# Optimization experiments

Hardware: AMD Instinct MI355X
Metric: run time of the kernel (lower is better)

Reference implementation:

```python
import jax, jax.numpy as jnp
import numpy as np

IN_DIM, H1, H2, H3, LATENT = 1024, 1024, 512, 256, 256
D, K, BETA = 32, 2048, 0.25
B = 16384


def _leaky(x):
    return jax.nn.leaky_relu(x, negative_slope=0.01)


def setup_inputs() -> dict:
    key = jax.random.key(0)
    ks = jax.random.split(key, 18)
    def lin(k, fan_in, fan_out):
        kw, kb = jax.random.split(k)
        s = 1.0 / np.sqrt(fan_in)
        W = jax.random.uniform(kw, (fan_in, fan_out), jnp.float32, -s, s)
        b = jax.random.uniform(kb, (fan_out,), jnp.float32, -s, s)
        return W, b
    We1, be1 = lin(ks[0], IN_DIM, H1)
    We2, be2 = lin(ks[1], H1, H2)
    We3, be3 = lin(ks[2], H2, H3)
    We4, be4 = lin(ks[3], H3, LATENT)
    Wd1, bd1 = lin(ks[4], LATENT, H3)
    Wd2, bd2 = lin(ks[5], H3, H2)
    Wd3, bd3 = lin(ks[6], H2, H1)
    Wd4, bd4 = lin(ks[7], H1, IN_DIM)
    E = jax.random.uniform(ks[8], (K, D), jnp.float32, -1.0 / K, 1.0 / K)  # codebook
    x = jax.random.uniform(ks[9], (B, IN_DIM), jnp.float32)
    return {"x": x, "We1": We1, "be1": be1, "We2": We2, "be2": be2,
            "We3": We3, "be3": be3, "We4": We4, "be4": be4, "E": E,
            "Wd1": Wd1, "bd1": bd1, "Wd2": Wd2, "bd2": bd2,
            "Wd3": Wd3, "bd3": bd3, "Wd4": Wd4, "bd4": bd4}


def reference(x, We1, be1, We2, be2, We3, be3, We4, be4, E,
              Wd1, bd1, Wd2, bd2, Wd3, bd3, Wd4, bd4):
    # encoder MLP
    h = _leaky(x @ We1 + be1)
    h = _leaky(h @ We2 + be2)
    h = _leaky(h @ We3 + be3)
    z = h @ We4 + be4                      # [B, LATENT]
    # vector quantizer
    zr = z.reshape(-1, D)                  # [N, D], N = B*LATENT/D
    dist = (jnp.sum(zr * zr, axis=1, keepdims=True)
            + jnp.sum(E * E, axis=1)
            - 2.0 * zr @ E.T)              # [N, K]
    idx = jnp.argmin(dist, axis=1)         # [N]
    # one-hot @ E == direct gather of nearest codebook rows
    q = E[idx].reshape(z.shape)            # [B, LATENT]
    commit = jnp.mean(jnp.sum(jnp.square(jax.lax.stop_gradient(q) - z), axis=1))
    embed = jnp.mean(jnp.sum(jnp.square(q - jax.lax.stop_gradient(z)), axis=1))
    vq_loss = BETA * commit + embed
    e = z + jax.lax.stop_gradient(q - z)   # straight-through
    # decoder MLP
    h = _leaky(e @ Wd1 + bd1)
    h = _leaky(h @ Wd2 + bd2)
    h = _leaky(h @ Wd3 + bd3)
    recon = jax.nn.sigmoid(h @ Wd4 + bd4)
    recon_loss = jnp.mean(jnp.sum(jnp.square(recon - x), axis=-1))
    loss = recon_loss + vq_loss
    return z, e, recon, loss, recon_loss, vq_loss
```

## Files before the change

### kernel.cpp

```cpp
#include <hip/hip_runtime.h>
#include <stdint.h>

typedef __attribute__((ext_vector_type(8))) _Float16 half8;
typedef __attribute__((ext_vector_type(4))) _Float16 half4;
typedef __attribute__((ext_vector_type(4))) float f32x4;

__device__ __forceinline__ void gload_lds16(const void* g, void* l) {
  __builtin_amdgcn_global_load_lds(
      (const __attribute__((address_space(1))) void*)g,
      (__attribute__((address_space(3))) void*)l, 16, 0, 0);
}

#define GBAR asm volatile("s_barrier" ::: "memory")
#define LGKM0                                            \
  asm volatile("s_waitcnt lgkmcnt(0)" ::: "memory");     \
  __builtin_amdgcn_sched_barrier(0)

#define MMA_Q(QM, QN)                                                        \
  __builtin_amdgcn_s_setprio(1);                                             \
  _Pragma("unroll") for (int s = 0; s < 2; s++)                              \
  _Pragma("unroll") for (int i = 0; i < 4; i++)                              \
  _Pragma("unroll") for (int j = 0; j < 2; j++)                              \
      acc[(QM) * 4 + i][(QN) * 2 + j] = __builtin_amdgcn_mfma_f32_16x16x32_f16( \
          af[i][s], bq[j][s], acc[(QM) * 4 + i][(QN) * 2 + j], 0, 0, 0);     \
  __builtin_amdgcn_s_setprio(0);

template <int EPI>
__global__ __launch_bounds__(512, 2) void gemm8p(
    const _Float16* __restrict__ A, const _Float16* __restrict__ Bt,
    const float* __restrict__ bias, _Float16* __restrict__ Ch,
    float* __restrict__ Cf, int M, int N, int Kd,
    const _Float16* __restrict__ Xref, float* __restrict__ lossAcc) {
  extern __shared__ __align__(16) char dyn[];

  const int tid = threadIdx.x;
  const int lane = tid & 63;
  const int wav = tid >> 6;
  const int wr = wav >> 2;
  const int wc = wav & 3;
  const int l15 = lane & 15;
  const int quad = lane >> 4;

  const int nx = gridDim.x;
  const int nwg = nx * (int)gridDim.y;
  int bid = (int)blockIdx.y * nx + (int)blockIdx.x;
  bid = (bid & 7) * (nwg >> 3) + (bid >> 3);
  const int shift = 31 - __clz(nx);
  const int m0 = (bid >> shift) * 256;
  const int n0 = (bid & (nx - 1)) * 256;

  f32x4 acc[8][4];
#pragma unroll
  for (int i = 0; i < 8; i++)
#pragma unroll
    for (int j = 0; j < 4; j++) acc[i][j] = (f32x4){0.f, 0.f, 0.f, 0.f};

  auto stageA = [&](int kt, int slot, int RB) {
    const int row = RB + (tid >> 3);
    const int ch = tid & 7;
    const int gm = m0 + ((row >> 6) & 1) * 128 + (row >> 7) * 64 + (row & 63);
    const int kc = (ch ^ (row & 7)) << 3;
    gload_lds16(A + (size_t)gm * Kd + kt + kc,
                dyn + slot * 65536 + row * 128 + ch * 16);
  };
  auto stageB = [&](int kt, int slot, int RB) {
    const int row = RB + (tid >> 3);
    const int ch = tid & 7;
    const int gn = n0 + ((row >> 5) & 3) * 64 + (row >> 7) * 32 + (row & 31);
    const int kc = (ch ^ (row & 7)) << 3;
    gload_lds16(Bt + (size_t)gn * Kd + kt + kc,
                dyn + slot * 65536 + 32768 + row * 128 + ch * 16);
  };

  half8 af[4][2], bq[2][2];
  auto dsA = [&](const _Float16* As, int qm) {
#pragma unroll
    for (int i = 0; i < 4; i++) {
      const int ra = qm * 128 + wr * 64 + i * 16 + l15;
#pragma unroll
      for (int s = 0; s < 2; s++)
        af[i][s] = *(const half8*)&As[ra * 64 + (((s * 4 + quad) ^ (ra & 7)) << 3)];
    }
  };
  auto dsB = [&](const _Float16* Bs, int qn) {
#pragma unroll
    for (int j = 0; j < 2; j++) {
      const int rb = qn * 128 + wc * 32 + j * 16 + l15;
#pragma unroll
      for (int s = 0; s < 2; s++)
        bq[j][s] = *(const half8*)&Bs[rb * 64 + (((s * 4 + quad) ^ (rb & 7)) << 3)];
    }
  };

  const int NT = Kd >> 6;

  stageA(0, 0, 0);
  stageA(0, 0, 64);
  stageA(0, 0, 128);
  stageA(0, 0, 192);
  stageB(0, 0, 0);
  stageB(0, 0, 64);
  stageB(0, 0, 128);
  stageB(0, 0, 192);
  stageA(64, 1, 0);
  stageA(64, 1, 64);
  stageB(64, 1, 128);
  stageB(64, 1, 192);
  stageA(64, 1, 128);
  stageA(64, 1, 192);
  asm volatile("s_waitcnt vmcnt(6)" ::: "memory");
  GBAR;

  for (int t = 0; t < NT; ++t) {
    const int slot = t & 1;
    const int nsl = slot ^ 1;
    const int kt1 = (t + 1) << 6;
    const int kt2 = (t + 2) << 6;
    const bool p1 = (t + 1) < NT;
    const bool s2 = (t + 2) < NT;
    const _Float16* As = (const _Float16*)(dyn + slot * 65536);
    const _Float16* Bs = (const _Float16*)(dyn + slot * 65536 + 32768);

    dsA(As, 0);
    dsB(Bs, 0);
    if (p1) { stageB(kt1, nsl, 0); stageB(kt1, nsl, 64); }
    GBAR;
    LGKM0;
    MMA_Q(0, 0);
    GBAR;
    dsB(Bs, 1);
    if (s2) { stageA(kt2, slot, 0); stageA(kt2, slot, 64); }
    GBAR;
    LGKM0;
    MMA_Q(0, 1);
    GBAR;
    dsA(As, 1);
    if (s2) { stageB(kt2, slot, 128); stageB(kt2, slot, 192); }
    GBAR;
    LGKM0;
    MMA_Q(1, 1);
    GBAR;
    dsB(Bs, 0);
    if (s2) { stageA(kt2, slot, 128); stageA(kt2, slot, 192); }
    GBAR;
    LGKM0;
    MMA_Q(1, 0);
    if (s2) {
      asm volatile("s_waitcnt vmcnt(6)" ::: "memory");
    } else {
      asm volatile("s_waitcnt vmcnt(0)" ::: "memory");
    }
    GBAR;
  }

  if (EPI == 2) {
    float lsum = 0.f;
    int colv[4];
    float bv[4];
#pragma unroll
    for (int ni = 0; ni < 4; ni++) {
      colv[ni] = n0 + wc * 64 + (ni >> 1) * 32 + (ni & 1) * 16 + l15;
      bv[ni] = bias[colv[ni]];
    }
    const int gr0 = m0 + wr * 128;
#pragma unroll
    for (int mi = 0; mi < 8; mi++) {
      const int row = gr0 + (mi >> 2) * 64 + (mi & 3) * 16 + quad * 4;
#pragma unroll
      for (int r = 0; r < 4; r++) {
        const size_t ro = (size_t)(row + r) * N;
#pragma unroll
        for (int ni = 0; ni < 4; ni++) {
          const size_t o = ro + colv[ni];
          const float sg = 1.f / (1.f + __expf(-(acc[mi][ni][r] + bv[ni])));
          Cf[o] = sg;
          const float d = sg - (float)Xref[o];
          lsum += d * d;
        }
      }
    }
    float* red = (float*)dyn;
    red[tid] = lsum;
    __syncthreads();
    for (int s = 256; s > 0; s >>= 1) {
      if (tid < s) red[tid] += red[tid + s];
      __syncthreads();
    }
    if (tid == 0) atomicAdd(lossAcc, red[0]);
  } else {
    float* eb = (float*)dyn;
#pragma unroll
    for (int p = 0; p < 4; p++) {
      __syncthreads();
      if (wr == (p >> 1)) {
#pragma unroll
        for (int mi2 = 0; mi2 < 4; mi2++) {
          const int mi = (p & 1) * 4 + mi2;
#pragma unroll
          for (int ni = 0; ni < 4; ni++)
#pragma unroll
            for (int r = 0; r < 4; r++) {
              const int rl = mi2 * 16 + quad * 4 + r;
              const int cl = wc * 64 + ni * 16 + l15;
              eb[rl * 256 + cl] = acc[mi][ni][r];
            }
        }
      }
      __syncthreads();
#pragma unroll
      for (int j = 0; j < 8; j++) {
        const int c = j * 512 + tid;
        const int rl = c >> 6;
        const int cl = (c & 63) * 4;
        const f32x4 v = *(const f32x4*)&eb[rl * 256 + cl];
        const int gcol = n0 + cl;
        const f32x4 bvv = *(const f32x4*)&bias[gcol];
        const size_t o = (size_t)(m0 + p * 64 + rl) * N + gcol;
        half4 h;
#pragma unroll
        for (int q = 0; q < 4; q++) {
          float tv = v[q] + bvv[q];
          tv = tv > 0.f ? tv : 0.01f * tv;
          h[q] = (_Float16)tv;
        }
        *(half4*)&Ch[o] = h;
      }
    }
  }
}

template <int EPI, int BM, int BN>
__global__ __launch_bounds__(256, ((BM + BN) >= 256 ? 2 : ((BM + BN) == 192 ? 3 : 4)))
void gemm_bt(
    const _Float16* __restrict__ A, const _Float16* __restrict__ Bt,
    const float* __restrict__ bias, _Float16* __restrict__ Ch,
    float* __restrict__ Cf, int M, int N, int Kd,
    const _Float16* __restrict__ Xref, float* __restrict__ lossAcc) {
  constexpr int WM = BM / 2, WN = BN / 2;
  constexpr int MF = WM / 16, NF = WN / 16;
  constexpr int CA = BM / 32, CB = BN / 32;
  constexpr int CHUNKS = CA + CB;
  constexpr int STAGE = (BM + BN) * 64;
  __shared__ __align__(16) _Float16 smem[2 * STAGE];
  float* red = (float*)smem + 64 * BN;

  const int tid = threadIdx.x;
  const int lane = tid & 63;
  const int wav = tid >> 6;
  const int nx = gridDim.x;
  const int nwg = nx * (int)gridDim.y;
  int bid = (int)blockIdx.y * nx + (int)blockIdx.x;
  bid = (bid & 7) * (nwg >> 3) + (bid >> 3);
  const int shift = 31 - __clz(nx);
  const int m0 = (bid >> shift) * BM;
  const int n0 = (bid & (nx - 1)) * BN;
  const int wm = (wav >> 1) * WM;
  const int wn = (wav & 1) * WN;
  const int l15 = lane & 15;
  const int quad = lane >> 4;

  f32x4 acc[MF][NF];
#pragma unroll
  for (int i = 0; i < MF; i++)
#pragma unroll
    for (int j = 0; j < NF; j++) acc[i][j] = (f32x4){0.f, 0.f, 0.f, 0.f};

  auto issue = [&](int kt, int b) {
    _Float16* As = smem + b * STAGE;
    _Float16* Bs = As + BM * 64;
#pragma unroll
    for (int j = 0; j < CA; j++) {
      const int ci = j * 256 + tid;
      const int row = ci >> 3;
      const int kc = ((ci & 7) ^ (row & 7)) << 3;
      gload_lds16(A + (size_t)(m0 + row) * Kd + kt + kc, &As[ci * 8]);
    }
#pragma unroll
    for (int j = 0; j < CB; j++) {
      const int ci = j * 256 + tid;
      const int row = ci >> 3;
      const int kc = ((ci & 7) ^ (row & 7)) << 3;
      gload_lds16(Bt + (size_t)(n0 + row) * Kd + kt + kc, &Bs[ci * 8]);
    }
  };

  int buf = 0;
  issue(0, 0);
  for (int kt = 0; kt < Kd; kt += 64) {
    if (kt + 64 < Kd) {
      issue(kt + 64, buf ^ 1);
      asm volatile("s_waitcnt vmcnt(%0)" ::"i"(CHUNKS) : "memory");
    } else {
      asm volatile("s_waitcnt vmcnt(0)" ::: "memory");
    }
    asm volatile("s_barrier" ::: "memory");

    const _Float16* As = smem + buf * STAGE;
    const _Float16* Bs = As + BM * 64;
#pragma unroll
    for (int s = 0; s < 2; s++) {
      half8 af[MF], bqv[NF];
#pragma unroll
      for (int i = 0; i < MF; i++) {
        const int ra = wm + i * 16 + l15;
        const int ca = (s * 4 + quad) ^ (ra & 7);
        af[i] = *(const half8*)&As[ra * 64 + ca * 8];
      }
#pragma unroll
      for (int i = 0; i < NF; i++) {
        const int rb = wn + i * 16 + l15;
        const int cb = (s * 4 + quad) ^ (rb & 7);
        bqv[i] = *(const half8*)&Bs[rb * 64 + cb * 8];
      }
#pragma unroll
      for (int mi = 0; mi < MF; mi++)
#pragma unroll
        for (int ni = 0; ni < NF; ni++)
          acc[mi][ni] = __builtin_amdgcn_mfma_f32_16x16x32_f16(af[mi], bqv[ni],
                                                               acc[mi][ni], 0, 0, 0);
    }
    asm volatile("s_barrier" ::: "memory");
    buf ^= 1;
  }

  float lsum = 0.f;
  float* eb = (float*)smem;
  constexpr int DIV = BN / 4;
#pragma unroll
  for (int p = 0; p < BM / 64; p++) {
    __syncthreads();
    if ((wm >> 6) == p) {
#pragma unroll
      for (int mi = 0; mi < MF; mi++)
#pragma unroll
        for (int ni = 0; ni < NF; ni++)
#pragma unroll
          for (int r = 0; r < 4; r++) {
            const int rl = (wm & 63) + mi * 16 + quad * 4 + r;
            const int cl = wn + ni * 16 + l15;
            eb[rl * BN + cl] = acc[mi][ni][r];
          }
    }
    __syncthreads();
#pragma unroll
    for (int j = 0; j < BN / 16; j++) {
      const int c = j * 256 + tid;
      const int rl = c / DIV;
      const int cl = (c % DIV) * 4;
      const f32x4 v = *(const f32x4*)&eb[rl * BN + cl];
      const int gcol = n0 + cl;
      const f32x4 bv = *(const f32x4*)&bias[gcol];
      const size_t o = (size_t)(m0 + p * 64 + rl) * N + gcol;
      if (EPI == 0) {
        half4 h;
#pragma unroll
        for (int q = 0; q < 4; q++) {
          float t = v[q] + bv[q];
          t = t > 0.f ? t : 0.01f * t;
          h[q] = (_Float16)t;
        }
        *(half4*)&Ch[o] = h;
      } else if (EPI == 1) {
        f32x4 t;
        half4 h;
#pragma unroll
        for (int q = 0; q < 4; q++) {
          t[q] = v[q] + bv[q];
          h[q] = (_Float16)t[q];
        }
        *(f32x4*)&Cf[o] = t;
        *(half4*)&Ch[o] = h;
      } else {
        const half4 xr = *(const half4*)&Xref[o];
        f32x4 sv;
#pragma unroll
        for (int q = 0; q < 4; q++) {
          const float s = 1.f / (1.f + __expf(-(v[q] + bv[q])));
          sv[q] = s;
          const float d = s - (float)xr[q];
          lsum += d * d;
        }
        *(f32x4*)&Cf[o] = sv;
      }
    }
  }
  if (EPI == 2) {
    __syncthreads();
    red[tid] = lsum;
    __syncthreads();
    for (int s = 128; s > 0; s >>= 1) {
      if (tid < s) red[tid] += red[tid + s];
      __syncthreads();
    }
    if (tid == 0) atomicAdd(lossAcc, red[0]);
  }
}

__global__ __launch_bounds__(256, 4) void vq_argmin(
    const _Float16* __restrict__ zh, const _Float16* __restrict__ Ehf,
    const float* __restrict__ E, const float* __restrict__ ek2,
    float* __restrict__ e_out, _Float16* __restrict__ eh_out,
    float* __restrict__ vq_acc) {
  __shared__ __align__(16) _Float16 Es[512 * 32];
  __shared__ float ek2s[512];
  __shared__ float z2s[128];
  __shared__ int idxs[128];
  __shared__ float vred[256];

  const int tid = threadIdx.x;
  const int lane = tid & 63;
  const int wav = tid >> 6;
  const int l15 = lane & 15;
  const int quad = lane >> 4;
  const int rbase = blockIdx.x * 128 + wav * 32;
  constexpr unsigned KEYMASK = 0xFFFFF800u;

  half8 zf[2];
  float z2p[2];
#pragma unroll
  for (int m = 0; m < 2; m++) {
    zf[m] = *(const half8*)(zh + ((size_t)(rbase + m * 16 + l15)) * 32 + quad * 8);
    float s = 0.f;
#pragma unroll
    for (int j = 0; j < 8; j++) {
      float v = (float)zf[m][j];
      s += v * v;
    }
    s += __shfl_xor(s, 16);
    s += __shfl_xor(s, 32);
    z2p[m] = s;
  }
  if (quad == 0) {
#pragma unroll
    for (int m = 0; m < 2; m++) z2s[wav * 32 + m * 16 + l15] = z2p[m];
  }

  float key[2][4];
#pragma unroll
  for (int m = 0; m < 2; m++)
#pragma unroll
    for (int r = 0; r < 4; r++) key[m][r] = 1e30f;

  for (int cb = 0; cb < 2048; cb += 512) {
    __syncthreads();
#pragma unroll
    for (int j = 0; j < 8; j++) {
      const int u = j * 256 + tid;
      gload_lds16(Ehf + (size_t)cb * 32 + u * 8, &Es[u * 8]);
    }
    if (tid < 128) gload_lds16(&ek2[cb + tid * 4], &ek2s[tid * 4]);
    __syncthreads();

    int idxv = cb + l15;
    for (int c16 = 0; c16 < 32; c16++) {
      const half8 ef = *(const half8*)&Es[(c16 * 64 + lane) * 8];
      const float e2 = ek2s[c16 * 16 + l15];
      const f32x4 cinit = (f32x4){e2, e2, e2, e2};
      f32x4 d0 = __builtin_amdgcn_mfma_f32_16x16x32_f16(zf[0], ef, cinit, 0, 0, 0);
      f32x4 d1 = __builtin_amdgcn_mfma_f32_16x16x32_f16(zf[1], ef, cinit, 0, 0, 0);
#pragma unroll
      for (int r = 0; r < 4; r++) {
        key[0][r] = fminf(key[0][r],
                          __uint_as_float((__float_as_uint(d0[r]) & KEYMASK) | idxv));
        key[1][r] = fminf(key[1][r],
                          __uint_as_float((__float_as_uint(d1[r]) & KEYMASK) | idxv));
      }
      idxv += 16;
    }
  }

#pragma unroll
  for (int off = 1; off < 16; off <<= 1)
#pragma unroll
    for (int m = 0; m < 2; m++)
#pragma unroll
      for (int r = 0; r < 4; r++)
        key[m][r] = fminf(key[m][r], __shfl_xor(key[m][r], off));

  float vpart = 0.f;
  if (l15 == 0) {
#pragma unroll
    for (int m = 0; m < 2; m++)
#pragma unroll
      for (int r = 0; r < 4; r++) {
        const unsigned kb = __float_as_uint(key[m][r]);
        const int rl = wav * 32 + m * 16 + quad * 4 + r;
        idxs[rl] = (int)(kb & 0x7FFu);
        vpart += z2s[rl] + __uint_as_float(kb & KEYMASK);
      }
  }
  vred[tid] = vpart;
  __syncthreads();
  for (int s = 128; s > 0; s >>= 1) {
    if (tid < s) vred[tid] += vred[tid + s];
    __syncthreads();
  }
  if (tid == 0) atomicAdd(vq_acc, vred[0]);

#pragma unroll
  for (int it = 0; it < 2; it++) {
    const int slot = it * 256 + tid;
    const int rowb = slot >> 2, part = slot & 3;
    const int idx = idxs[rowb];
    const size_t orow = ((size_t)blockIdx.x * 128 + rowb) * 32 + part * 8;
    const f32x4 ea = *(const f32x4*)(E + (size_t)idx * 32 + part * 8);
    const f32x4 ebv = *(const f32x4*)(E + (size_t)idx * 32 + part * 8 + 4);
    *(f32x4*)(e_out + orow) = ea;
    *(f32x4*)(e_out + orow + 4) = ebv;
    half8 ehv;
#pragma unroll
    for (int j = 0; j < 4; j++) {
      ehv[j] = (_Float16)ea[j];
      ehv[j + 4] = (_Float16)ebv[j];
    }
    *(half8*)(eh_out + orow) = ehv;
  }
}

struct PrepArgs {
  const float* W[8];
  _Float16* Wt[8];
  int Kw[8], Nw[8];
  int base[9];
  const float* x;
  _Float16* xh;
  const float* E;
  _Float16* Ehf;
  float* ek2;
};

__global__ __launch_bounds__(256) void prep_k(PrepArgs a) {
  __shared__ float t[32][33];
  const int b = blockIdx.x;
  const int tid = threadIdx.x;
  if (b < 8192) {
    const size_t i = (size_t)b * 256 + tid;
    const f32x4 va = *(const f32x4*)(a.x + i * 8);
    const f32x4 vb = *(const f32x4*)(a.x + i * 8 + 4);
    half8 h;
#pragma unroll
    for (int j = 0; j < 4; j++) {
      h[j] = (_Float16)va[j];
      h[j + 4] = (_Float16)vb[j];
    }
    *(half8*)(a.xh + i * 8) = h;
    return;
  }
  if (b < 8192 + 3456) {
    int l = b - 8192;
    int w = 0;
    while (l >= a.base[w + 1]) w++;
    l -= a.base[w];
    const float* W = a.W[w];
    _Float16* Wt = a.Wt[w];
    const int K = a.Kw[w], N = a.Nw[w];
    const int nb = N >> 5;
    const int bx = (l % nb) * 32, by = (l / nb) * 32;
    const int tx = tid & 31, ty = tid >> 5;
#pragma unroll
    for (int i = 0; i < 32; i += 8)
      t[ty + i][tx] = W[(size_t)(by + ty + i) * N + bx + tx];
    __syncthreads();
#pragma unroll
    for (int i = 0; i < 32; i += 8)
      Wt[(size_t)(bx + ty + i) * K + by + tx] = (_Float16)t[tx][ty + i];
    return;
  }
  const int c = (b - 8192 - 3456) * 256 + tid;
  float s = 0.f;
#pragma unroll
  for (int k = 0; k < 32; k++) {
    const float v = a.E[(size_t)c * 32 + k];
    s += v * v;
    a.Ehf[(size_t)((c >> 4) * 64 + (k >> 3) * 16 + (c & 15)) * 8 + (k & 7)] =
        (_Float16)(-2.f * v);
  }
  a.ek2[c] = s;
}

__global__ void finalize_k(const float* __restrict__ scal, float* __restrict__ out) {
  const float vq = 1.25f * (scal[0] / 16384.f);
  const float rl = scal[1] / 16384.f;
  out[0] = rl + vq;
  out[1] = rl;
  out[2] = vq;
}

extern "C" void kernel_launch(void* const* d_in, const int* in_sizes, int n_in,
                              void* d_out, int out_size, void* d_ws, size_t ws_size,
                              hipStream_t stream) {
  const float* x = (const float*)d_in[0];
  const float* be1 = (const float*)d_in[2];
  const float* be2 = (const float*)d_in[4];
  const float* be3 = (const float*)d_in[6];
  const float* be4 = (const float*)d_in[8];
  const float* E = (const float*)d_in[9];
  const float* bd1 = (const float*)d_in[11];
  const float* bd2 = (const float*)d_in[13];
  const float* bd3 = (const float*)d_in[15];
  const float* bd4 = (const float*)d_in[17];

  float* out = (float*)d_out;
  char* ws = (char*)d_ws;

  size_t off = 0;
  auto alloc = [&](size_t bytes) {
    size_t r = off;
    off += (bytes + 255) & ~(size_t)255;
    return r;
  };
  const size_t oXH = alloc((size_t)16384 * 1024 * 2);
  const size_t oWT1 = alloc((size_t)1024 * 1024 * 2);
  const size_t oWT2 = alloc((size_t)512 * 1024 * 2);
  const size_t oWT3 = alloc((size_t)256 * 512 * 2);
  const size_t oWT4 = alloc((size_t)256 * 256 * 2);
  const size_t oWD1 = alloc((size_t)256 * 256 * 2);
  const size_t oWD2 = alloc((size_t)512 * 256 * 2);
  const size_t oWD3 = alloc((size_t)1024 * 512 * 2);
  const size_t oWD4 = alloc((size_t)1024 * 1024 * 2);
  const size_t oEHF = alloc((size_t)2048 * 32 * 2);
  const size_t oEK2 = alloc((size_t)2048 * 4);
  const size_t oSC = alloc(256);
  const size_t oZH = alloc((size_t)16384 * 256 * 2);
  const size_t oQH = alloc((size_t)16384 * 256 * 2);
  const size_t oH1 = alloc((size_t)16384 * 1024 * 2);
  const size_t oH2 = alloc((size_t)16384 * 512 * 2);
  const size_t oH3 = alloc((size_t)16384 * 256 * 2);

  _Float16* xh = (_Float16*)(ws + oXH);
  _Float16* WT1 = (_Float16*)(ws + oWT1);
  _Float16* WT2 = (_Float16*)(ws + oWT2);
  _Float16* WT3 = (_Float16*)(ws + oWT3);
  _Float16* WT4 = (_Float16*)(ws + oWT4);
  _Float16* WD1 = (_Float16*)(ws + oWD1);
  _Float16* WD2 = (_Float16*)(ws + oWD2);
  _Float16* WD3 = (_Float16*)(ws + oWD3);
  _Float16* WD4 = (_Float16*)(ws + oWD4);
  _Float16* Ehf = (_Float16*)(ws + oEHF);
  float* ek2 = (float*)(ws + oEK2);
  float* scal = (float*)(ws + oSC);
  _Float16* zhw = (_Float16*)(ws + oZH);
  _Float16* qh = (_Float16*)(ws + oQH);
  _Float16* h1 = (_Float16*)(ws + oH1);
  _Float16* h2 = (_Float16*)(ws + oH2);
  _Float16* h3 = (_Float16*)(ws + oH3);

  float* zout = out;
  float* eout = out + (size_t)16384 * 256;
  float* rout = out + (size_t)16384 * 256 * 2;
  float* sout = rout + (size_t)16384 * 1024;

  hipMemsetAsync(ws + oSC, 0, 8, stream);

  hipFuncSetAttribute((const void*)gemm8p<0>,
                      hipFuncAttributeMaxDynamicSharedMemorySize, 131072);
  hipFuncSetAttribute((const void*)gemm8p<2>,
                      hipFuncAttributeMaxDynamicSharedMemorySize, 131072);

  PrepArgs pa;
  pa.W[0] = (const float*)d_in[1];  pa.Wt[0] = WT1; pa.Kw[0] = 1024; pa.Nw[0] = 1024;
  pa.W[1] = (const float*)d_in[3];  pa.Wt[1] = WT2; pa.Kw[1] = 1024; pa.Nw[1] = 512;
  pa.W[2] = (const float*)d_in[5];  pa.Wt[2] = WT3; pa.Kw[2] = 512;  pa.Nw[2] = 256;
  pa.W[3] = (const float*)d_in[7];  pa.Wt[3] = WT4; pa.Kw[3] = 256;  pa.Nw[3] = 256;
  pa.W[4] = (const float*)d_in[10]; pa.Wt[4] = WD1; pa.Kw[4] = 256;  pa.Nw[4] = 256;
  pa.W[5] = (const float*)d_in[12]; pa.Wt[5] = WD2; pa.Kw[5] = 256;  pa.Nw[5] = 512;
  pa.W[6] = (const float*)d_in[14]; pa.Wt[6] = WD3; pa.Kw[6] = 512;  pa.Nw[6] = 1024;
  pa.W[7] = (const float*)d_in[16]; pa.Wt[7] = WD4; pa.Kw[7] = 1024; pa.Nw[7] = 1024;
  int acc = 0;
  for (int w = 0; w < 8; w++) {
    pa.base[w] = acc;
    acc += (pa.Kw[w] >> 5) * (pa.Nw[w] >> 5);
  }
  pa.base[8] = acc;
  pa.x = x; pa.xh = xh; pa.E = E; pa.Ehf = Ehf; pa.ek2 = ek2;

  dim3 blk(256);
  prep_k<<<8192 + 3456 + 8, blk, 0, stream>>>(pa);

  gemm8p<0><<<dim3(4, 64), dim3(512), 131072, stream>>>(
      xh, WT1, be1, h1, nullptr, 16384, 1024, 1024, nullptr, nullptr);
  gemm_bt<0, 128, 128><<<dim3(4, 128), blk, 0, stream>>>(
      h1, WT2, be2, h2, nullptr, 16384, 512, 1024, nullptr, nullptr);
  gemm_bt<0, 64, 64><<<dim3(4, 256), blk, 0, stream>>>(
      h2, WT3, be3, h3, nullptr, 16384, 256, 512, nullptr, nullptr);
  gemm_bt<1, 64, 64><<<dim3(4, 256), blk, 0, stream>>>(
      h3, WT4, be4, zhw, zout, 16384, 256, 256, nullptr, nullptr);
  vq_argmin<<<1024, blk, 0, stream>>>(zhw, Ehf, E, ek2, eout, qh, &scal[0]);
  gemm_bt<0, 64, 64><<<dim3(4, 256), blk, 0, stream>>>(
      qh, WD1, bd1, h3, nullptr, 16384, 256, 256, nullptr, nullptr);
  gemm_bt<0, 128, 128><<<dim3(4, 128), blk, 0, stream>>>(
      h3, WD2, bd2, h2, nullptr, 16384, 512, 256, nullptr, nullptr);
  gemm8p<0><<<dim3(4, 64), dim3(512), 131072, stream>>>(
      h2, WD3, bd3, h1, nullptr, 16384, 1024, 512, nullptr, nullptr);
  gemm8p<2><<<dim3(4, 64), dim3(512), 131072, stream>>>(
      h1, WD4, bd4, nullptr, rout, 16384, 1024, 1024, xh, &scal[1]);
  finalize_k<<<1, 1, 0, stream>>>(scal, sout);
}
```

Before: 396.0 us.

## Keep both B fragment halves in registers to drop a reload and a barrier phase

Result: no change. 390.6 us (-1.4%).

```diff
diff --git a/kernel.cpp b/kernel.cpp
--- a/kernel.cpp
+++ b/kernel.cpp
@@ -16,13 +16,13 @@
   asm volatile("s_waitcnt lgkmcnt(0)" ::: "memory");     \
   __builtin_amdgcn_sched_barrier(0)
 
-#define MMA_Q(QM, QN)                                                        \
+#define MMA_Q(QM, QN, BQ)                                                    \
   __builtin_amdgcn_s_setprio(1);                                             \
   _Pragma("unroll") for (int s = 0; s < 2; s++)                              \
   _Pragma("unroll") for (int i = 0; i < 4; i++)                              \
   _Pragma("unroll") for (int j = 0; j < 2; j++)                              \
       acc[(QM) * 4 + i][(QN) * 2 + j] = __builtin_amdgcn_mfma_f32_16x16x32_f16( \
-          af[i][s], bq[j][s], acc[(QM) * 4 + i][(QN) * 2 + j], 0, 0, 0);     \
+          af[i][s], BQ[j][s], acc[(QM) * 4 + i][(QN) * 2 + j], 0, 0, 0);     \
   __builtin_amdgcn_s_setprio(0);
 
 template <int EPI>
@@ -72,7 +72,7 @@
                 dyn + slot * 65536 + 32768 + row * 128 + ch * 16);
   };
 
-  half8 af[4][2], bq[2][2];
+  half8 af[4][2], bq0[2][2], bq1[2][2];
   auto dsA = [&](const _Float16* As, int qm) {
 #pragma unroll
     for (int i = 0; i < 4; i++) {
@@ -82,13 +82,22 @@
         af[i][s] = *(const half8*)&As[ra * 64 + (((s * 4 + quad) ^ (ra & 7)) << 3)];
     }
   };
-  auto dsB = [&](const _Float16* Bs, int qn) {
+  auto dsB0 = [&](const _Float16* Bs) {
 #pragma unroll
     for (int j = 0; j < 2; j++) {
-      const int rb = qn * 128 + wc * 32 + j * 16 + l15;
+      const int rb = wc * 32 + j * 16 + l15;
 #pragma unroll
       for (int s = 0; s < 2; s++)
-        bq[j][s] = *(const half8*)&Bs[rb * 64 + (((s * 4 + quad) ^ (rb & 7)) << 3)];
+        bq0[j][s] = *(const half8*)&Bs[rb * 64 + (((s * 4 + quad) ^ (rb & 7)) << 3)];
+    }
+  };
+  auto dsB1 = [&](const _Float16* Bs) {
+#pragma unroll
+    for (int j = 0; j < 2; j++) {
+      const int rb = 128 + wc * 32 + j * 16 + l15;
+#pragma unroll
+      for (int s = 0; s < 2; s++)
+        bq1[j][s] = *(const half8*)&Bs[rb * 64 + (((s * 4 + quad) ^ (rb & 7)) << 3)];
     }
   };
 
@@ -96,19 +105,17 @@
 
   stageA(0, 0, 0);
   stageA(0, 0, 64);
+  stageB(0, 0, 128);
+  stageB(0, 0, 192);
   stageA(0, 0, 128);
   stageA(0, 0, 192);
   stageB(0, 0, 0);
   stageB(0, 0, 64);
-  stageB(0, 0, 128);
-  stageB(0, 0, 192);
   stageA(64, 1, 0);
   stageA(64, 1, 64);
   stageB(64, 1, 128);
   stageB(64, 1, 192);
-  stageA(64, 1, 128);
-  stageA(64, 1, 192);
-  asm volatile("s_waitcnt vmcnt(6)" ::: "memory");
+  asm volatile("s_waitcnt vmcnt(4)" ::: "memory");
   GBAR;
 
   for (int t = 0; t < NT; ++t) {
@@ -117,36 +124,33 @@
     const int kt1 = (t + 1) << 6;
     const int kt2 = (t + 2) << 6;
     const bool p1 = (t + 1) < NT;
-    const bool s2 = (t + 2) < NT;
+    const bool p2 = (t + 2) < NT;
     const _Float16* As = (const _Float16*)(dyn + slot * 65536);
     const _Float16* Bs = (const _Float16*)(dyn + slot * 65536 + 32768);
 
     dsA(As, 0);
-    dsB(Bs, 0);
+    dsB0(Bs);
+    if (p1) { stageA(kt1, nsl, 128); stageA(kt1, nsl, 192); }
+    GBAR;
+    LGKM0;
+    MMA_Q(0, 0, bq0);
+    GBAR;
+    dsB1(Bs);
     if (p1) { stageB(kt1, nsl, 0); stageB(kt1, nsl, 64); }
     GBAR;
     LGKM0;
-    MMA_Q(0, 0);
+    MMA_Q(0, 1, bq1);
     GBAR;
-    dsB(Bs, 1);
-    if (s2) { stageA(kt2, slot, 0); stageA(kt2, slot, 64); }
+    dsA(As, 1);
+    if (p2) { stageA(kt2, slot, 0); stageA(kt2, slot, 64); }
     GBAR;
     LGKM0;
-    MMA_Q(0, 1);
+    MMA_Q(1, 1, bq1);
     GBAR;
-    dsA(As, 1);
-    if (s2) { stageB(kt2, slot, 128); stageB(kt2, slot, 192); }
-    GBAR;
-    LGKM0;
-    MMA_Q(1, 1);
-    GBAR;
-    dsB(Bs, 0);
-    if (s2) { stageA(kt2, slot, 128); stageA(kt2, slot, 192); }
-    GBAR;
-    LGKM0;
-    MMA_Q(1, 0);
-    if (s2) {
-      asm volatile("s_waitcnt vmcnt(6)" ::: "memory");
+    if (p2) { stageB(kt2, slot, 128); stageB(kt2, slot, 192); }
+    MMA_Q(1, 0, bq0);
+    if (p2) {
+      asm volatile("s_waitcnt vmcnt(4)" ::: "memory");
     } else {
       asm volatile("s_waitcnt vmcnt(0)" ::: "memory");
     }
```
